# Optimization experiments

Hardware: AMD Instinct MI355X
Metric: run time of the kernel (lower is better)

Reference implementation:

```python
import jax, jax.numpy as jnp
import numpy as np

B, N, F_IN, F_OUT = 8, 2048, 256, 256
NEG_SLOPE = 0.2
EPS = 1e-7


def setup_inputs() -> dict:
    key = jax.random.key(0)
    k1, k2, k3, k4, k5 = jax.random.split(key, 5)
    x = jax.random.normal(k1, (B, N, F_IN), dtype=jnp.float32)
    # A is a 0/1 adjacency mask used as float in the module
    A = jax.random.bernoulli(k2, 0.5, (B, N, N)).astype(jnp.float32)
    # W: xavier_normal_ init, shape [in_features, out_features]
    W = jax.random.normal(k3, (F_IN, F_OUT), dtype=jnp.float32) * np.sqrt(2.0 / (F_IN + F_OUT))
    # attention_mechanism: Linear(2*F_OUT, 1) -> weight vector [2*F_OUT], scalar bias
    bound = 1.0 / np.sqrt(2 * F_OUT)
    a_w = jax.random.uniform(k4, (2 * F_OUT,), dtype=jnp.float32, minval=-bound, maxval=bound)
    a_b = jax.random.uniform(k5, (), dtype=jnp.float32, minval=-bound, maxval=bound)
    return {"A": A, "x": x, "W": W, "a_w": a_w, "a_b": a_b}


def reference(A, x, W, a_w, a_b):
    # Wh = x @ W : [B, N, F_OUT]
    Wh = jnp.einsum('bnf,fo->bno', x, W)
    # Linear([Wh_i ; Wh_j]) == Wh_i @ a_w[:F] + Wh_j @ a_w[F:] + b  (no O(N^2 F) concat)
    s_src = Wh @ a_w[:F_OUT]   # [B, N] contribution of row index i
    s_dst = Wh @ a_w[F_OUT:]   # [B, N] contribution of col index j
    e = s_src[:, :, None] + s_dst[:, None, :] + a_b  # [B, N, N]
    e = jnp.where(e > 0, e, NEG_SLOPE * e)           # leaky_relu(0.2)
    # masked softmax over dim=1 (as in the original module)
    exps = jnp.exp(e) * A
    sums = jnp.sum(exps, axis=1, keepdims=True) + EPS
    attn = exps / sums                                # [B, N, N]
    return jnp.einsum('bij,bjo->bio', attn, Wh)       # [B, N, F_OUT]
```

## Files before the change

### kernel.cpp

```cpp
#include <hip/hip_runtime.h>
#include <hip/hip_bf16.h>

#define NN 2048
#define BB 8
#define FD 256
#define NEG_SLOPE 0.2f
#define EPSV 1e-7f

typedef __bf16 bf16x8 __attribute__((ext_vector_type(8)));
typedef __bf16 bf16x4 __attribute__((ext_vector_type(4)));
typedef float f32x4 __attribute__((ext_vector_type(4)));

__device__ __forceinline__ void gload16(const __bf16* g, __bf16* l) {
    __builtin_amdgcn_global_load_lds((const __attribute__((address_space(1))) unsigned int*)g,
                                     (__attribute__((address_space(3))) unsigned int*)l,
                                     16, 0, 0);
}

__global__ __launch_bounds__(256) void k1_prep(const float* __restrict__ W,
                                               __bf16* __restrict__ WT) {
    int idx = blockIdx.x * 256 + threadIdx.x;
    int o = idx >> 8, f = idx & 255;
    WT[idx] = (__bf16)W[f * FD + o];
}

__global__ __launch_bounds__(256) void k2_whgemm(const float* __restrict__ x,
                                                 const __bf16* __restrict__ WT,
                                                 const float* __restrict__ a_w,
                                                 float* __restrict__ Wh,
                                                 float* __restrict__ s_src,
                                                 float* __restrict__ s_dst) {
    const int wave = threadIdx.x >> 6;
    const int lane = threadIdx.x & 63;
    const int row0 = blockIdx.x * 32 + (wave >> 1) * 16;
    const int ohalf = (wave & 1) * 128;
    const int m = lane & 15;
    const int quad = lane >> 4;
    const int row = row0 + m;
    const float* xrow = x + (size_t)row * FD + quad * 8;

    f32x4 acc[8];
#pragma unroll
    for (int n = 0; n < 8; ++n) acc[n] = (f32x4){0.f, 0.f, 0.f, 0.f};

    for (int k0 = 0; k0 < FD; k0 += 32) {
        float4 xa = *(const float4*)(xrow + k0);
        float4 xb = *(const float4*)(xrow + k0 + 4);
        bf16x8 af;
        af[0] = (__bf16)xa.x; af[1] = (__bf16)xa.y; af[2] = (__bf16)xa.z; af[3] = (__bf16)xa.w;
        af[4] = (__bf16)xb.x; af[5] = (__bf16)xb.y; af[6] = (__bf16)xb.z; af[7] = (__bf16)xb.w;
#pragma unroll
        for (int n = 0; n < 8; ++n) {
            int o = ohalf + n * 16 + m;
            bf16x8 bf = *(const bf16x8*)(WT + o * FD + k0 + quad * 8);
            acc[n] = __builtin_amdgcn_mfma_f32_16x16x32_bf16(af, bf, acc[n], 0, 0, 0);
        }
    }
#pragma unroll
    for (int n = 0; n < 8; ++n) {
        int o = ohalf + n * 16 + m;
#pragma unroll
        for (int r = 0; r < 4; ++r) {
            Wh[(size_t)(row0 + quad * 4 + r) * FD + o] = acc[n][r];
        }
    }

    float psrc[4] = {0.f, 0.f, 0.f, 0.f};
    float pdst[4] = {0.f, 0.f, 0.f, 0.f};
#pragma unroll
    for (int n = 0; n < 8; ++n) {
        int o = ohalf + n * 16 + m;
        float awS = a_w[o], awD = a_w[FD + o];
#pragma unroll
        for (int r = 0; r < 4; ++r) {
            psrc[r] += acc[n][r] * awS;
            pdst[r] += acc[n][r] * awD;
        }
    }
#pragma unroll
    for (int off = 1; off <= 8; off <<= 1) {
#pragma unroll
        for (int r = 0; r < 4; ++r) {
            psrc[r] += __shfl_xor(psrc[r], off, 64);
            pdst[r] += __shfl_xor(pdst[r], off, 64);
        }
    }
    __shared__ float sS[2][2][16], sD[2][2][16];
    if (m == 0) {
        int rp = wave >> 1, oh = wave & 1;
#pragma unroll
        for (int r = 0; r < 4; ++r) {
            sS[rp][oh][quad * 4 + r] = psrc[r];
            sD[rp][oh][quad * 4 + r] = pdst[r];
        }
    }
    __syncthreads();
    if (threadIdx.x < 32) {
        int rp = threadIdx.x >> 4, idx = threadIdx.x & 15;
        int orow = blockIdx.x * 32 + rp * 16 + idx;
        s_src[orow] = sS[rp][0][idx] + sS[rp][1][idx];
        s_dst[orow] = sD[rp][0][idx] + sD[rp][1][idx];
    }
}

__global__ __launch_bounds__(256) void k4_den(const float* __restrict__ A,
                                              const float* __restrict__ s_src,
                                              const float* __restrict__ s_dst,
                                              const float* __restrict__ a_bp,
                                              float* __restrict__ den_part) {
    const int blk = blockIdx.x;
    const int b = blk & 7;
    const int jhalf = (blk >> 3) & 1;
    const int isp = blk >> 4;
    const int i0 = isp * 32;
    const int j = jhalf * 1024 + threadIdx.x * 4;
    __shared__ float ss[32];
    if (threadIdx.x < 32) ss[threadIdx.x] = s_src[b * NN + i0 + threadIdx.x] + a_bp[0];
    __syncthreads();
    float4 sd = *(const float4*)(s_dst + b * NN + j);
    float ax = 0.f, ay = 0.f, az = 0.f, aw = 0.f;
    const float* Ap = A + ((size_t)b * NN + i0) * NN + j;
#pragma unroll 8
    for (int i = 0; i < 32; ++i) {
        float4 a = *(const float4*)(Ap + (size_t)i * NN);
        float si = ss[i];
        float e0 = si + sd.x; e0 = e0 > 0.f ? e0 : NEG_SLOPE * e0;
        float e1 = si + sd.y; e1 = e1 > 0.f ? e1 : NEG_SLOPE * e1;
        float e2 = si + sd.z; e2 = e2 > 0.f ? e2 : NEG_SLOPE * e2;
        float e3 = si + sd.w; e3 = e3 > 0.f ? e3 : NEG_SLOPE * e3;
        ax += a.x * __expf(e0);
        ay += a.y * __expf(e1);
        az += a.z * __expf(e2);
        aw += a.w * __expf(e3);
    }
    float4 r = (float4){ax, ay, az, aw};
    *(float4*)(den_part + (size_t)isp * (BB * NN) + b * NN + j) = r;
}

__global__ __launch_bounds__(256) void k5_wht(const float* __restrict__ Wh,
                                              const float* __restrict__ den_part,
                                              __bf16* __restrict__ WhT) {
    const int b = blockIdx.z;
    const int j0 = blockIdx.x * 64;
    const int o0 = blockIdx.y * 64;
    __shared__ float tile[64][65];
    __shared__ float invd[64];
    if (threadIdx.x < 64) {
        float s = 0.f;
        const float* dp = den_part + b * NN + j0 + threadIdx.x;
#pragma unroll 8
        for (int sI = 0; sI < 64; ++sI) s += dp[(size_t)sI * (BB * NN)];
        invd[threadIdx.x] = 1.f / (s + EPSV);
    }
    __syncthreads();
    int jr = threadIdx.x >> 4, oc = (threadIdx.x & 15) * 4;
#pragma unroll
    for (int p = 0; p < 4; ++p) {
        int jj = jr + p * 16;
        float4 v = *(const float4*)(Wh + (size_t)(b * NN + j0 + jj) * FD + o0 + oc);
        float s = invd[jj];
        tile[jj][oc + 0] = v.x * s;
        tile[jj][oc + 1] = v.y * s;
        tile[jj][oc + 2] = v.z * s;
        tile[jj][oc + 3] = v.w * s;
    }
    __syncthreads();
    int ow = threadIdx.x >> 4, jc = (threadIdx.x & 15) * 4;
#pragma unroll
    for (int p = 0; p < 4; ++p) {
        int o = ow + p * 16;
        bf16x4 wv;
        wv[0] = (__bf16)tile[jc + 0][o];
        wv[1] = (__bf16)tile[jc + 1][o];
        wv[2] = (__bf16)tile[jc + 2][o];
        wv[3] = (__bf16)tile[jc + 3][o];
        *(bf16x4*)(WhT + (size_t)(b * FD + o0 + o) * NN + j0 + jc) = wv;
    }
}

__global__ __launch_bounds__(256) void k6f(const float* __restrict__ A,
                                           const __bf16* __restrict__ WhT,
                                           const float* __restrict__ s_src,
                                           const float* __restrict__ s_dst,
                                           const float* __restrict__ a_bp,
                                           float* __restrict__ out) {
    __shared__ __bf16 lP[2][64 * 64];
    __shared__ __bf16 lB[2][128 * 64];
    const int blk = blockIdx.x;
    const int b = blk & 7;
    const int r_ = blk >> 3;
    const int nh = r_ & 1;
    const int mt = r_ >> 1;
    const int i0 = mt * 64;
    const int o0 = nh * 128;
    const int t = threadIdx.x;
    const int w = t >> 6, lane = t & 63;
    const int m = lane & 15, quad = lane >> 4;
    const int wr = w >> 1, wc = w & 1;

    const int srow = lane >> 3;
    const int schunk = (lane & 7) ^ srow;
    const __bf16* gB = WhT + ((size_t)(b * FD + o0 + w * 8 + srow)) * NN + schunk * 8;

#define STAGEB(buf, step) { \
        const __bf16* gb = gB + (step) * 64; \
        gload16(gb,                   &lB[buf][0] + (w * 8) * 64); \
        gload16(gb + (size_t)32 * NN, &lB[buf][0] + (32 + w * 8) * 64); \
        gload16(gb + (size_t)64 * NN, &lB[buf][0] + (64 + w * 8) * 64); \
        gload16(gb + (size_t)96 * NN, &lB[buf][0] + (96 + w * 8) * 64); \
    }

    const int pr = t >> 2;
    const int pc = (t & 3) * 16;
    const float ssr = s_src[b * NN + i0 + pr] + a_bp[0];
    const float* Ap  = A + ((size_t)(b * NN + i0 + pr)) * NN + pc;
    const float* sdp = s_dst + b * NN + pc;
    const int ch0 = pc >> 3;
    const int sw0 = ((ch0    ) ^ (pr & 7)) * 8;
    const int sw1 = ((ch0 + 1) ^ (pr & 7)) * 8;
    __bf16* lProw = &lP[0][0] + pr * 64;

    float4 a0_, a1_, a2_, a3_, d0_, d1_, d2_, d3_;
#define LOADP(step) { \
        const float* ap = Ap  + (step) * 64; \
        const float* dp = sdp + (step) * 64; \
        a0_ = *(const float4*)(ap + 0);  a1_ = *(const float4*)(ap + 4); \
        a2_ = *(const float4*)(ap + 8);  a3_ = *(const float4*)(ap + 12); \
        d0_ = *(const float4*)(dp + 0);  d1_ = *(const float4*)(dp + 4); \
        d2_ = *(const float4*)(dp + 8);  d3_ = *(const float4*)(dp + 12); \
    }
#define PB1(vv, idx, av, dv) { \
        float e = ssr + dv; e = e > 0.f ? e : NEG_SLOPE * e; \
        vv[idx] = (__bf16)(av * __expf(e)); }
#define PBUILD(buf) { \
        bf16x8 v0, v1; \
        PB1(v0, 0, a0_.x, d0_.x) PB1(v0, 1, a0_.y, d0_.y) \
        PB1(v0, 2, a0_.z, d0_.z) PB1(v0, 3, a0_.w, d0_.w) \
        PB1(v0, 4, a1_.x, d1_.x) PB1(v0, 5, a1_.y, d1_.y) \
        PB1(v0, 6, a1_.z, d1_.z) PB1(v0, 7, a1_.w, d1_.w) \
        PB1(v1, 0, a2_.x, d2_.x) PB1(v1, 1, a2_.y, d2_.y) \
        PB1(v1, 2, a2_.z, d2_.z) PB1(v1, 3, a2_.w, d2_.w) \
        PB1(v1, 4, a3_.x, d3_.x) PB1(v1, 5, a3_.y, d3_.y) \
        PB1(v1, 6, a3_.z, d3_.z) PB1(v1, 7, a3_.w, d3_.w) \
        *(bf16x8*)(lProw + (buf) * 4096 + sw0) = v0; \
        *(bf16x8*)(lProw + (buf) * 4096 + sw1) = v1; \
    }

    LOADP(0)
    STAGEB(0, 0)
    PBUILD(0)

    f32x4 acc[2][4];
#pragma unroll
    for (int mi = 0; mi < 2; ++mi)
#pragma unroll
        for (int n = 0; n < 4; ++n) acc[mi][n] = (f32x4){0.f, 0.f, 0.f, 0.f};

    const int swz = (m & 7) * 8;
    for (int kt = 0; kt < 32; ++kt) {
        __syncthreads();
        const int cur = kt & 1, nb = cur ^ 1;
        if (kt < 31) {
            LOADP(kt + 1)
            STAGEB(nb, kt + 1)
        }
        const __bf16* lPc = &lP[cur][0];
        const __bf16* lBc = &lB[cur][0];
#pragma unroll
        for (int ks = 0; ks < 2; ++ks) {
            const int kof = (ks * 32 + quad * 8) ^ swz;
            bf16x8 pa0 = *(const bf16x8*)(lPc + (wr * 32 + m) * 64 + kof);
            bf16x8 pa1 = *(const bf16x8*)(lPc + (wr * 32 + 16 + m) * 64 + kof);
#pragma unroll
            for (int n = 0; n < 4; ++n) {
                bf16x8 bfr = *(const bf16x8*)(lBc + (wc * 64 + n * 16 + m) * 64 + kof);
                acc[0][n] = __builtin_amdgcn_mfma_f32_16x16x32_bf16(pa0, bfr, acc[0][n], 0, 0, 0);
                acc[1][n] = __builtin_amdgcn_mfma_f32_16x16x32_bf16(pa1, bfr, acc[1][n], 0, 0, 0);
            }
        }
        if (kt < 31) PBUILD(nb)
    }

#pragma unroll
    for (int mi = 0; mi < 2; ++mi)
#pragma unroll
        for (int n = 0; n < 4; ++n) {
            int o = o0 + wc * 64 + n * 16 + m;
#pragma unroll
            for (int rr = 0; rr < 4; ++rr) {
                int orow = i0 + wr * 32 + mi * 16 + quad * 4 + rr;
                out[((size_t)b * NN + orow) * FD + o] = acc[mi][n][rr];
            }
        }
#undef STAGEB
#undef LOADP
#undef PB1
#undef PBUILD
}

extern "C" void kernel_launch(void* const* d_in, const int* in_sizes, int n_in,
                              void* d_out, int out_size, void* d_ws, size_t ws_size,
                              hipStream_t stream) {
    const float* A   = (const float*)d_in[0];
    const float* x   = (const float*)d_in[1];
    const float* W   = (const float*)d_in[2];
    const float* a_w = (const float*)d_in[3];
    const float* a_b = (const float*)d_in[4];
    float* out = (float*)d_out;

    char* ws = (char*)d_ws;
    __bf16* WT      = (__bf16*)ws;
    float*  Wh      = (float*)(ws + 131072);
    __bf16* WhT     = (__bf16*)(ws + 16908288);
    float*  s_src   = (float*)(ws + 25296896);
    float*  s_dst   = (float*)(ws + 25362432);
    float*  den_part= (float*)(ws + 25427968);

    k1_prep<<<256, 256, 0, stream>>>(W, WT);
    k2_whgemm<<<512, 256, 0, stream>>>(x, WT, a_w, Wh, s_src, s_dst);
    k4_den<<<1024, 256, 0, stream>>>(A, s_src, s_dst, a_b, den_part);
    k5_wht<<<dim3(32, 4, 8), 256, 0, stream>>>(Wh, den_part, WhT);
    k6f<<<512, 256, 0, stream>>>(A, WhT, s_src, s_dst, a_b, out);
}
```

Baseline: 295.7 us.

## Fuse all stages into one cooperative persistent kernel with grid syncs

Merges the five separate kernels into a single cooperative launch of 512 blocks that runs each stage in turn, separated by grid-wide barriers, with a fallback to the multi-kernel path if the cooperative launch fails. The aim is to remove per-kernel launch gaps and tail drain between stages. In exchange, it relies on all 512 blocks being co-resident, which the launch bound of 2 blocks per SM targets. The shared LDS use of the merged stages and the grid barriers may lower occupancy and add sync overhead.

```diff
diff --git a/kernel.cpp b/kernel.cpp
--- a/kernel.cpp
+++ b/kernel.cpp
@@ -1,5 +1,8 @@
 #include <hip/hip_runtime.h>
 #include <hip/hip_bf16.h>
+#include <hip/hip_cooperative_groups.h>
+
+namespace cg = cooperative_groups;
 
 #define NN 2048
 #define BB 8
@@ -17,22 +20,17 @@
                                      16, 0, 0);
 }
 
-__global__ __launch_bounds__(256) void k1_prep(const float* __restrict__ W,
-                                               __bf16* __restrict__ WT) {
-    int idx = blockIdx.x * 256 + threadIdx.x;
-    int o = idx >> 8, f = idx & 255;
-    WT[idx] = (__bf16)W[f * FD + o];
-}
-
-__global__ __launch_bounds__(256) void k2_whgemm(const float* __restrict__ x,
-                                                 const __bf16* __restrict__ WT,
-                                                 const float* __restrict__ a_w,
-                                                 float* __restrict__ Wh,
-                                                 float* __restrict__ s_src,
-                                                 float* __restrict__ s_dst) {
+
+__device__ __forceinline__ void d_k2(int bid,
+                                     const float* __restrict__ x,
+                                     const __bf16* __restrict__ WT,
+                                     const float* __restrict__ a_w,
+                                     float* __restrict__ Wh,
+                                     float* __restrict__ s_src,
+                                     float* __restrict__ s_dst) {
     const int wave = threadIdx.x >> 6;
     const int lane = threadIdx.x & 63;
-    const int row0 = blockIdx.x * 32 + (wave >> 1) * 16;
+    const int row0 = bid * 32 + (wave >> 1) * 16;
     const int ohalf = (wave & 1) * 128;
     const int m = lane & 15;
     const int quad = lane >> 4;
@@ -97,24 +95,25 @@
     __syncthreads();
     if (threadIdx.x < 32) {
         int rp = threadIdx.x >> 4, idx = threadIdx.x & 15;
-        int orow = blockIdx.x * 32 + rp * 16 + idx;
+        int orow = bid * 32 + rp * 16 + idx;
         s_src[orow] = sS[rp][0][idx] + sS[rp][1][idx];
         s_dst[orow] = sD[rp][0][idx] + sD[rp][1][idx];
     }
 }
 
-__global__ __launch_bounds__(256) void k4_den(const float* __restrict__ A,
-                                              const float* __restrict__ s_src,
-                                              const float* __restrict__ s_dst,
-                                              const float* __restrict__ a_bp,
-                                              float* __restrict__ den_part) {
-    const int blk = blockIdx.x;
+__device__ __forceinline__ void d_k4(int blk,
+                                     const float* __restrict__ A,
+                                     const float* __restrict__ s_src,
+                                     const float* __restrict__ s_dst,
+                                     const float* __restrict__ a_bp,
+                                     float* __restrict__ den_part) {
     const int b = blk & 7;
     const int jhalf = (blk >> 3) & 1;
     const int isp = blk >> 4;
     const int i0 = isp * 32;
     const int j = jhalf * 1024 + threadIdx.x * 4;
     __shared__ float ss[32];
+    __syncthreads();
     if (threadIdx.x < 32) ss[threadIdx.x] = s_src[b * NN + i0 + threadIdx.x] + a_bp[0];
     __syncthreads();
     float4 sd = *(const float4*)(s_dst + b * NN + j);
@@ -137,12 +136,13 @@
     *(float4*)(den_part + (size_t)isp * (BB * NN) + b * NN + j) = r;
 }
 
-__global__ __launch_bounds__(256) void k5_wht(const float* __restrict__ Wh,
-                                              const float* __restrict__ den_part,
-                                              __bf16* __restrict__ WhT) {
-    const int b = blockIdx.z;
-    const int j0 = blockIdx.x * 64;
-    const int o0 = blockIdx.y * 64;
+__device__ __forceinline__ void d_k5(int lb,
+                                     const float* __restrict__ Wh,
+                                     const float* __restrict__ den_part,
+                                     __bf16* __restrict__ WhT) {
+    const int j0 = (lb & 31) * 64;
+    const int o0 = ((lb >> 5) & 3) * 64;
+    const int b = lb >> 7;
     __shared__ float tile[64][65];
     __shared__ float invd[64];
     if (threadIdx.x < 64) {
@@ -178,15 +178,15 @@
     }
 }
 
-__global__ __launch_bounds__(256) void k6f(const float* __restrict__ A,
-                                           const __bf16* __restrict__ WhT,
-                                           const float* __restrict__ s_src,
-                                           const float* __restrict__ s_dst,
-                                           const float* __restrict__ a_bp,
-                                           float* __restrict__ out) {
+__device__ __forceinline__ void d_k6f(int blk,
+                                      const float* __restrict__ A,
+                                      const __bf16* __restrict__ WhT,
+                                      const float* __restrict__ s_src,
+                                      const float* __restrict__ s_dst,
+                                      const float* __restrict__ a_bp,
+                                      float* __restrict__ out) {
     __shared__ __bf16 lP[2][64 * 64];
     __shared__ __bf16 lB[2][128 * 64];
-    const int blk = blockIdx.x;
     const int b = blk & 7;
     const int r_ = blk >> 3;
     const int nh = r_ & 1;
@@ -298,6 +298,75 @@
 #undef PBUILD
 }
 
+__global__ __launch_bounds__(256, 2) void kmega(const float* __restrict__ A,
+                                                const float* __restrict__ x,
+                                                const float* __restrict__ W,
+                                                const float* __restrict__ a_w,
+                                                const float* __restrict__ a_bp,
+                                                float* __restrict__ out,
+                                                __bf16* __restrict__ WT,
+                                                float* __restrict__ Wh,
+                                                __bf16* __restrict__ WhT,
+                                                float* __restrict__ s_src,
+                                                float* __restrict__ s_dst,
+                                                float* __restrict__ den_part) {
+    cg::grid_group grid = cg::this_grid();
+    const int bid = blockIdx.x;
+
+    if (bid < 256) {
+        int idx = bid * 256 + threadIdx.x;
+        int o = idx >> 8, f = idx & 255;
+        WT[idx] = (__bf16)W[f * FD + o];
+    }
+    grid.sync();
+
+    d_k2(bid, x, WT, a_w, Wh, s_src, s_dst);
+    grid.sync();
+
+    for (int lb = bid; lb < 1024; lb += 512) d_k4(lb, A, s_src, s_dst, a_bp, den_part);
+    grid.sync();
+
+    for (int lb = bid; lb < 1024; lb += 512) d_k5(lb, Wh, den_part, WhT);
+    grid.sync();
+
+    d_k6f(bid, A, WhT, s_src, s_dst, a_bp, out);
+}
+
+__global__ __launch_bounds__(256) void k1_prep(const float* __restrict__ W,
+                                               __bf16* __restrict__ WT) {
+    int idx = blockIdx.x * 256 + threadIdx.x;
+    int o = idx >> 8, f = idx & 255;
+    WT[idx] = (__bf16)W[f * FD + o];
+}
+__global__ __launch_bounds__(256) void k2_whgemm(const float* __restrict__ x,
+                                                 const __bf16* __restrict__ WT,
+                                                 const float* __restrict__ a_w,
+                                                 float* __restrict__ Wh,
+                                                 float* __restrict__ s_src,
+                                                 float* __restrict__ s_dst) {
+    d_k2(blockIdx.x, x, WT, a_w, Wh, s_src, s_dst);
+}
+__global__ __launch_bounds__(256) void k4_den(const float* __restrict__ A,
+                                              const float* __restrict__ s_src,
+                                              const float* __restrict__ s_dst,
+                                              const float* __restrict__ a_bp,
+                                              float* __restrict__ den_part) {
+    d_k4(blockIdx.x, A, s_src, s_dst, a_bp, den_part);
+}
+__global__ __launch_bounds__(256) void k5_wht(const float* __restrict__ Wh,
+                                              const float* __restrict__ den_part,
+                                              __bf16* __restrict__ WhT) {
+    d_k5(blockIdx.x, Wh, den_part, WhT);
+}
+__global__ __launch_bounds__(256) void k6f(const float* __restrict__ A,
+                                           const __bf16* __restrict__ WhT,
+                                           const float* __restrict__ s_src,
+                                           const float* __restrict__ s_dst,
+                                           const float* __restrict__ a_bp,
+                                           float* __restrict__ out) {
+    d_k6f(blockIdx.x, A, WhT, s_src, s_dst, a_bp, out);
+}
+
 extern "C" void kernel_launch(void* const* d_in, const int* in_sizes, int n_in,
                               void* d_out, int out_size, void* d_ws, size_t ws_size,
                               hipStream_t stream) {
@@ -316,9 +385,18 @@
     float*  s_dst   = (float*)(ws + 25362432);
     float*  den_part= (float*)(ws + 25427968);
 
-    k1_prep<<<256, 256, 0, stream>>>(W, WT);
-    k2_whgemm<<<512, 256, 0, stream>>>(x, WT, a_w, Wh, s_src, s_dst);
-    k4_den<<<1024, 256, 0, stream>>>(A, s_src, s_dst, a_b, den_part);
-    k5_wht<<<dim3(32, 4, 8), 256, 0, stream>>>(Wh, den_part, WhT);
-    k6f<<<512, 256, 0, stream>>>(A, WhT, s_src, s_dst, a_b, out);
-}
+    void* kargs[] = {
+        (void*)&A, (void*)&x, (void*)&W, (void*)&a_w, (void*)&a_b, (void*)&out,
+        (void*)&WT, (void*)&Wh, (void*)&WhT, (void*)&s_src, (void*)&s_dst, (void*)&den_part
+    };
+    hipError_t err = hipLaunchCooperativeKernel(reinterpret_cast<void*>(kmega),
+                                                dim3(512), dim3(256), kargs, 0, stream);
+    if (err != hipSuccess) {
+        (void)hipGetLastError();
+        k1_prep<<<256, 256, 0, stream>>>(W, WT);
+        k2_whgemm<<<512, 256, 0, stream>>>(x, WT, a_w, Wh, s_src, s_dst);
+        k4_den<<<1024, 256, 0, stream>>>(A, s_src, s_dst, a_b, den_part);
+        k5_wht<<<1024, 256, 0, stream>>>(Wh, den_part, WhT);
+        k6f<<<512, 256, 0, stream>>>(A, WhT, s_src, s_dst, a_b, out);
+    }
+}
```

Measured after the change: 543.6 us. +83.8%, slower.
